# Optimization experiments

Measured on AMD Instinct MI355X. Metric: run time of the kernel, lower is better.

The kernel has to match this reference:

```python
import jax, jax.numpy as jnp
import numpy as np

B, T, C = 2, 4096, 1024
H = 16            # n_head (== n_groups == n_kv_heads)
HD = C // H       # head_dim = 64
W = 256           # window_size
ROPE_BASE = 10000.0


def _rope(x):
    # x: (B, H, T, HD); rotate interleaved pairs with position along axis 2
    t = x.shape[2]
    inv_freq = 1.0 / (ROPE_BASE ** (jnp.arange(0, HD, 2, dtype=jnp.float32) / HD))  # (HD/2,)
    freqs = jnp.arange(t, dtype=jnp.float32)[:, None] * inv_freq[None, :]           # (T, HD/2)
    cos = jnp.cos(freqs)[None, None].astype(x.dtype)
    sin = jnp.sin(freqs)[None, None].astype(x.dtype)
    x1, x2 = x[..., 0::2], x[..., 1::2]
    o1 = x1 * cos - x2 * sin
    o2 = x1 * sin + x2 * cos
    return jnp.stack([o1, o2], axis=-1).reshape(x.shape)


def setup_inputs() -> dict:
    key = jax.random.key(0)
    ks = jax.random.split(key, 5)
    s = 1.0 / np.sqrt(C)
    return {
        "x": jax.random.normal(ks[0], (B, T, C), dtype=jnp.float32),
        "wq": jax.random.normal(ks[1], (C, C), dtype=jnp.float32) * s,
        "wk": jax.random.normal(ks[2], (C, C), dtype=jnp.float32) * s,
        "wv": jax.random.normal(ks[3], (C, C), dtype=jnp.float32) * s,
        "wo": jax.random.normal(ks[4], (C, C), dtype=jnp.float32) * s,
    }


def reference(x, wq, wk, wv, wo):
    # projections (Linear stores (out, in) -> x @ w.T)
    q = jnp.einsum('btc,oc->bto', x, wq).reshape(B, T, H, HD).transpose(0, 2, 1, 3)
    k = jnp.einsum('btc,oc->bto', x, wk).reshape(B, T, H, HD).transpose(0, 2, 1, 3)
    v = jnp.einsum('btc,oc->bto', x, wv).reshape(B, T, H, HD).transpose(0, 2, 1, 3)

    q = _rope(q)
    k = _rope(k)

    nW = T // W
    qw = q.reshape(B, H, nW, W, HD)
    kw = k.reshape(B, H, nW, W, HD)
    vw = v.reshape(B, H, nW, W, HD)

    scale = 1.0 / jnp.sqrt(jnp.asarray(HD, dtype=q.dtype))
    att = jnp.einsum('bhnqd,bhnkd->bhnqk', qw, kw) * scale   # per-window, no causal mask
    att = jax.nn.softmax(att, axis=-1)
    yw = jnp.einsum('bhnqk,bhnkd->bhnqd', att, vw)

    y = yw.reshape(B, H, T, HD).transpose(0, 2, 1, 3).reshape(B, T, C)
    return jnp.einsum('btc,oc->bto', y, wo)
```

## Files before the change

### kernel.cpp

```cpp
#include <hip/hip_runtime.h>
#include <math.h>

typedef float f32x4 __attribute__((ext_vector_type(4)));
typedef __bf16 bf16x8 __attribute__((ext_vector_type(8)));
typedef unsigned short ushort_t;

#define MFMA16(a, b, c) __builtin_amdgcn_mfma_f32_16x16x32_bf16((a), (b), (c), 0, 0, 0)

static __device__ __forceinline__ ushort_t f2bf(float f) {
  union { float f; unsigned u; } v; v.f = f;
  unsigned u = v.u;
  return (ushort_t)((u + 0x7FFFu + ((u >> 16) & 1u)) >> 16);
}
static __device__ __forceinline__ float bf2f(ushort_t h) {
  union { unsigned u; float f; } v; v.u = ((unsigned)h) << 16;
  return v.f;
}
static __device__ __forceinline__ void gl_lds16(const void* g, void* lds_uniform) {
  __builtin_amdgcn_global_load_lds(
      (const __attribute__((address_space(1))) unsigned int*)g,
      (__attribute__((address_space(3))) unsigned int*)lds_uniform, 16, 0, 0);
}

__global__ void prep(const float* __restrict__ x,
                     const float* __restrict__ wq, const float* __restrict__ wk,
                     const float* __restrict__ wv, const float* __restrict__ wo,
                     ushort_t* __restrict__ Xb, ushort_t* __restrict__ Wqb,
                     ushort_t* __restrict__ Wkb, ushort_t* __restrict__ Wvb,
                     ushort_t* __restrict__ Wob, float2* __restrict__ cs) {
  const int bid = blockIdx.x;
  if (bid < 12288) {
    const float* src;
    ushort_t* dst;
    int i;
    if (bid < 8192) {
      src = x; dst = Xb;
      i = bid * 256 + threadIdx.x;
    } else {
      const int wi = (bid - 8192) >> 10;
      src = (wi == 0) ? wq : (wi == 1) ? wk : (wi == 2) ? wv : wo;
      dst = (wi == 0) ? Wqb : (wi == 1) ? Wkb : (wi == 2) ? Wvb : Wob;
      i = ((bid - 8192) & 1023) * 256 + threadIdx.x;
    }
    f32x4 v = ((const f32x4*)src)[i];
    ushort4 o;
    o.x = f2bf(v.x); o.y = f2bf(v.y); o.z = f2bf(v.z); o.w = f2bf(v.w);
    ((ushort4*)dst)[i] = o;
  } else {
    int idx = (bid - 12288) * 256 + threadIdx.x;
    int pos = idx >> 5, i = idx & 31;
    float inv = exp2f(-(float)i * 0.41524101f);
    float th = (float)pos * inv;
    float s, c;
    sincosf(th, &s, &c);
    cs[idx] = make_float2(c, s);
  }
}

template <int OUTBF>
__global__ __launch_bounds__(256) void gemm_nt(
    const ushort_t* __restrict__ A,
    const ushort_t* __restrict__ W0, const ushort_t* __restrict__ W1, const ushort_t* __restrict__ W2,
    void* __restrict__ C0, void* __restrict__ C1, void* __restrict__ C2,
    int K, int N) {
  __shared__ __align__(16) ushort_t As[128 * 64];
  __shared__ __align__(16) ushort_t Bs[128 * 64];
  const int z = blockIdx.z;
  const ushort_t* W = (z == 0) ? W0 : (z == 1 ? W1 : W2);
  void* Cv = (z == 0) ? C0 : (z == 1 ? C1 : C2);

  const int t = threadIdx.x;
  const int lane = t & 63;
  const int l15 = lane & 15;
  const int quad = lane >> 4;
  const int wave = t >> 6;
  const int wm = wave & 1, wn = wave >> 1;
  const int bm = blockIdx.x, bn = blockIdx.y;

  const int srow = t >> 3;
  const int schunk = (t & 7) ^ (srow & 7);
  const ushort_t* Ag = A + (size_t)(bm * 128 + srow) * K + schunk * 8;
  const ushort_t* Wg = W + (size_t)(bn * 128 + srow) * K + schunk * 8;
  char* AsB = (char*)As + (t & 192) * 16;
  char* BsB = (char*)Bs + (t & 192) * 16;
  const size_t rK = (size_t)32 * K;

  const f32x4 zero4 = {0.f, 0.f, 0.f, 0.f};
  f32x4 acc[4][4];
#pragma unroll
  for (int i = 0; i < 4; ++i)
#pragma unroll
    for (int j = 0; j < 4; ++j) acc[i][j] = zero4;

  for (int kt = 0; kt < K; kt += 64) {
#pragma unroll
    for (int p = 0; p < 4; ++p) {
      gl_lds16(Ag + p * rK + kt, AsB + p * 4096);
      gl_lds16(Wg + p * rK + kt, BsB + p * 4096);
    }
    __syncthreads();
#pragma unroll
    for (int ks = 0; ks < 2; ++ks) {
      bf16x8 af[4], bfr[4];
#pragma unroll
      for (int i = 0; i < 4; ++i) {
        const int r = wm * 64 + i * 16 + l15;
        af[i] = *(const bf16x8*)&As[r * 64 + (((ks * 4 + quad) ^ (r & 7)) * 8)];
      }
#pragma unroll
      for (int j = 0; j < 4; ++j) {
        const int r = wn * 64 + j * 16 + l15;
        bfr[j] = *(const bf16x8*)&Bs[r * 64 + (((ks * 4 + quad) ^ (r & 7)) * 8)];
      }
#pragma unroll
      for (int i = 0; i < 4; ++i)
#pragma unroll
        for (int j = 0; j < 4; ++j) acc[i][j] = MFMA16(af[i], bfr[j], acc[i][j]);
    }
    __syncthreads();
  }

  const int rbase = bm * 128 + wm * 64 + quad * 4;
  const int cbase = bn * 128 + wn * 64 + l15;
#pragma unroll
  for (int i = 0; i < 4; ++i)
#pragma unroll
    for (int j = 0; j < 4; ++j)
#pragma unroll
      for (int r = 0; r < 4; ++r) {
        size_t idx = (size_t)(rbase + i * 16 + r) * N + (cbase + j * 16);
        if (OUTBF)
          ((ushort_t*)Cv)[idx] = f2bf(acc[i][j][r]);
        else
          ((float*)Cv)[idx] = acc[i][j][r];
      }
}

static __device__ __forceinline__ void rope8(const ushort_t* __restrict__ g,
                                             ushort_t* __restrict__ lds,
                                             const float2* __restrict__ cs4, float scale) {
  uint4 raw = *(const uint4*)g;
  unsigned rw[4] = {raw.x, raw.y, raw.z, raw.w};
  ushort_t o[8];
#pragma unroll
  for (int m = 0; m < 4; ++m) {
    float x1 = bf2f((ushort_t)(rw[m] & 0xffffu));
    float x2 = bf2f((ushort_t)(rw[m] >> 16));
    float2 sc = cs4[m];
    o[2 * m]     = f2bf((x1 * sc.x - x2 * sc.y) * scale);
    o[2 * m + 1] = f2bf((x1 * sc.y + x2 * sc.x) * scale);
  }
  uint4 w;
  w.x = (unsigned)o[0] | ((unsigned)o[1] << 16);
  w.y = (unsigned)o[2] | ((unsigned)o[3] << 16);
  w.z = (unsigned)o[4] | ((unsigned)o[5] << 16);
  w.w = (unsigned)o[6] | ((unsigned)o[7] << 16);
  *(uint4*)lds = w;
}

static __device__ __forceinline__ bf16x8 rope_frag(const ushort_t* __restrict__ g,
                                                   const float2* __restrict__ cs4,
                                                   float scale) {
  uint4 raw = *(const uint4*)g;
  unsigned rw[4] = {raw.x, raw.y, raw.z, raw.w};
  union { unsigned u[4]; bf16x8 v; } out;
#pragma unroll
  for (int m = 0; m < 4; ++m) {
    float x1 = bf2f((ushort_t)(rw[m] & 0xffffu));
    float x2 = bf2f((ushort_t)(rw[m] >> 16));
    float2 sc = cs4[m];
    float o0 = (x1 * sc.x - x2 * sc.y) * scale;
    float o1 = (x1 * sc.y + x2 * sc.x) * scale;
    out.u[m] = (unsigned)f2bf(o0) | ((unsigned)f2bf(o1) << 16);
  }
  return out.v;
}

__global__ __launch_bounds__(256) void attn(
    const ushort_t* __restrict__ Qb, const ushort_t* __restrict__ Kb,
    const ushort_t* __restrict__ Vb, ushort_t* __restrict__ Yb,
    const float2* __restrict__ cs) {
  __shared__ __align__(16) ushort_t smem[26112];
  ushort_t* Ks = smem;
  ushort_t* Vt = smem;
  ushort_t* Pc = smem + 16896;

  const int t = threadIdx.x;
  const int lane = t & 63, wave = t >> 6;
  const int l15 = lane & 15, quad = lane >> 4;
  const int win = blockIdx.x >> 1, slice = blockIdx.x & 1;
  const int h = blockIdx.y, b = blockIdx.z;
  const int kBase = win * 256, qBase = kBase + slice * 128;
  const size_t gbase = ((size_t)b * 4096) * 1024 + h * 64;

  const int sr = t >> 3;
  const int c0 = (t & 7) * 8;
  const int qw = wave * 32;

#pragma unroll
  for (int p = 0; p < 8; ++p) {
    int r = p * 32 + sr;
    rope8(Kb + gbase + (size_t)(kBase + r) * 1024 + c0, Ks + r * 72 + c0,
          cs + (size_t)(kBase + r) * 32 + (c0 >> 1), 1.0f);
  }

  bf16x8 qf[2][2];
#pragma unroll
  for (int i = 0; i < 2; ++i)
#pragma unroll
    for (int ks = 0; ks < 2; ++ks) {
      int row = qBase + qw + i * 16 + l15;
      int col = ks * 32 + quad * 8;
      qf[i][ks] = rope_frag(Qb + gbase + (size_t)row * 1024 + col,
                            cs + (size_t)row * 32 + (col >> 1), 0.125f);
    }
  __syncthreads();

  uint4 vr[8];
#pragma unroll
  for (int p = 0; p < 8; ++p)
    vr[p] = *(const uint4*)(Vb + gbase + (size_t)(kBase + p * 32 + sr) * 1024 + c0);

  const f32x4 zero4 = {0.f, 0.f, 0.f, 0.f};
  f32x4 ST[2][16];
#pragma unroll
  for (int i = 0; i < 2; ++i)
#pragma unroll
    for (int kt = 0; kt < 16; ++kt) ST[i][kt] = zero4;
#pragma unroll
  for (int ks = 0; ks < 2; ++ks)
#pragma unroll
    for (int kt = 0; kt < 16; ++kt) {
      bf16x8 kf = *(const bf16x8*)&Ks[(kt * 16 + l15) * 72 + ks * 32 + quad * 8];
      ST[0][kt] = MFMA16(kf, qf[0][ks], ST[0][kt]);
      ST[1][kt] = MFMA16(kf, qf[1][ks], ST[1][kt]);
    }

  float mx[2], linv[2];
#pragma unroll
  for (int i = 0; i < 2; ++i) {
    float m = ST[i][0][0];
#pragma unroll
    for (int kt = 0; kt < 16; ++kt)
#pragma unroll
      for (int r = 0; r < 4; ++r) m = fmaxf(m, ST[i][kt][r]);
    m = fmaxf(m, __shfl_xor(m, 16));
    m = fmaxf(m, __shfl_xor(m, 32));
    mx[i] = m;
  }
  unsigned Pp[2][16][2];
#pragma unroll
  for (int i = 0; i < 2; ++i) {
    float sum = 0.f;
#pragma unroll
    for (int kt = 0; kt < 16; ++kt) {
      float e0 = __expf(ST[i][kt][0] - mx[i]);
      float e1 = __expf(ST[i][kt][1] - mx[i]);
      float e2 = __expf(ST[i][kt][2] - mx[i]);
      float e3 = __expf(ST[i][kt][3] - mx[i]);
      sum += (e0 + e1) + (e2 + e3);
      Pp[i][kt][0] = (unsigned)f2bf(e0) | ((unsigned)f2bf(e1) << 16);
      Pp[i][kt][1] = (unsigned)f2bf(e2) | ((unsigned)f2bf(e3) << 16);
    }
    sum += __shfl_xor(sum, 16);
    sum += __shfl_xor(sum, 32);
    linv[i] = 1.0f / sum;
  }

  __syncthreads();

#pragma unroll
  for (int p = 0; p < 8; ++p) {
    int k = p * 32 + sr;
    ushort_t vv[8];
    vv[0] = vr[p].x & 0xffffu; vv[1] = vr[p].x >> 16;
    vv[2] = vr[p].y & 0xffffu; vv[3] = vr[p].y >> 16;
    vv[4] = vr[p].z & 0xffffu; vv[5] = vr[p].z >> 16;
    vv[6] = vr[p].w & 0xffffu; vv[7] = vr[p].w >> 16;
#pragma unroll
    for (int e = 0; e < 8; ++e) {
      int ee = (e + (t & 7)) & 7;
      Vt[(c0 + ee) * 264 + k] = vv[ee];
    }
  }

  auto writeP = [&](int kc) {
#pragma unroll
    for (int i = 0; i < 2; ++i)
#pragma unroll
      for (int jt = 0; jt < 4; ++jt) {
        uint2 w = make_uint2(Pp[i][kc * 4 + jt][0], Pp[i][kc * 4 + jt][1]);
        *(uint2*)&Pc[(qw + i * 16 + l15) * 72 + jt * 16 + quad * 4] = w;
      }
  };

  writeP(0);
  __syncthreads();

  f32x4 O[2][4];
#pragma unroll
  for (int i = 0; i < 2; ++i)
#pragma unroll
    for (int jd = 0; jd < 4; ++jd) O[i][jd] = zero4;

#pragma unroll
  for (int kc = 0; kc < 4; ++kc) {
#pragma unroll
    for (int ks = 0; ks < 2; ++ks) {
      bf16x8 a0 = *(const bf16x8*)&Pc[(qw + l15) * 72 + ks * 32 + quad * 8];
      bf16x8 a1 = *(const bf16x8*)&Pc[(qw + 16 + l15) * 72 + ks * 32 + quad * 8];
#pragma unroll
      for (int jd = 0; jd < 4; ++jd) {
        bf16x8 bv = *(const bf16x8*)&Vt[(jd * 16 + l15) * 264 + kc * 64 + ks * 32 + quad * 8];
        O[0][jd] = MFMA16(a0, bv, O[0][jd]);
        O[1][jd] = MFMA16(a1, bv, O[1][jd]);
      }
    }
    if (kc < 3) writeP(kc + 1);
  }

  float lv[2][4];
#pragma unroll
  for (int i = 0; i < 2; ++i)
#pragma unroll
    for (int r = 0; r < 4; ++r) lv[i][r] = __shfl(linv[i], quad * 4 + r);
#pragma unroll
  for (int i = 0; i < 2; ++i)
#pragma unroll
    for (int jd = 0; jd < 4; ++jd)
#pragma unroll
      for (int r = 0; r < 4; ++r) {
        int row = qBase + qw + i * 16 + quad * 4 + r;
        int col = jd * 16 + l15;
        Yb[gbase + (size_t)row * 1024 + col] = f2bf(O[i][jd][r] * lv[i][r]);
      }
}

extern "C" void kernel_launch(void* const* d_in, const int* in_sizes, int n_in,
                              void* d_out, int out_size, void* d_ws, size_t ws_size,
                              hipStream_t stream) {
  (void)in_sizes; (void)n_in; (void)out_size; (void)ws_size;
  const float* x  = (const float*)d_in[0];
  const float* wq = (const float*)d_in[1];
  const float* wk = (const float*)d_in[2];
  const float* wv = (const float*)d_in[3];
  const float* wo = (const float*)d_in[4];

  char* ws = (char*)d_ws;
  ushort_t* Xb  = (ushort_t*)(ws);
  ushort_t* Wqb = (ushort_t*)(ws + 16777216);
  ushort_t* Wkb = Wqb + 1048576;
  ushort_t* Wvb = Wkb + 1048576;
  ushort_t* Wob = Wvb + 1048576;
  ushort_t* Qb  = (ushort_t*)(ws + 25165824);
  ushort_t* Kb  = Qb + 8388608;
  ushort_t* Vb  = Kb + 8388608;
  ushort_t* Yb  = Vb + 8388608;
  float2*   cs  = (float2*)(ws + 92274688);

  prep<<<dim3(12800), dim3(256), 0, stream>>>(x, wq, wk, wv, wo,
                                              Xb, Wqb, Wkb, Wvb, Wob, cs);

  gemm_nt<1><<<dim3(64, 8, 3), dim3(256), 0, stream>>>(
      Xb, Wqb, Wkb, Wvb, (void*)Qb, (void*)Kb, (void*)Vb, 1024, 1024);

  attn<<<dim3(32, 16, 2), dim3(256), 0, stream>>>(Qb, Kb, Vb, Yb, cs);

  gemm_nt<0><<<dim3(64, 8, 1), dim3(256), 0, stream>>>(
      Yb, Wob, Wob, Wob, d_out, d_out, d_out, 1024, 1024);
}
```

Baseline: 220.4 us.

## Split attention work across 8 waves with 16 query rows each

The attention kernel now launches 512 threads per block, so each wave handles 16 query rows instead of 32. This halves per-thread register state (score tiles, P fragments, accumulators) and the per-thread K/V load and rope work. The V global loads are also moved after the softmax so the V registers are not live during the QK phase. The intent is more waves in flight to hide latency, at the cost of more barrier participants and less reuse of each K/V fragment per wave.

```diff
diff --git a/kernel.cpp b/kernel.cpp
--- a/kernel.cpp
+++ b/kernel.cpp
@@ -176,7 +176,7 @@
   return out.v;
 }
 
-__global__ __launch_bounds__(256) void attn(
+__global__ __launch_bounds__(512, 4) void attn(
     const ushort_t* __restrict__ Qb, const ushort_t* __restrict__ Kb,
     const ushort_t* __restrict__ Vb, ushort_t* __restrict__ Yb,
     const float2* __restrict__ cs) {
@@ -195,83 +195,72 @@
 
   const int sr = t >> 3;
   const int c0 = (t & 7) * 8;
-  const int qw = wave * 32;
-
-#pragma unroll
-  for (int p = 0; p < 8; ++p) {
-    int r = p * 32 + sr;
+  const int qw = wave * 16;
+
+#pragma unroll
+  for (int p = 0; p < 4; ++p) {
+    int r = p * 64 + sr;
     rope8(Kb + gbase + (size_t)(kBase + r) * 1024 + c0, Ks + r * 72 + c0,
           cs + (size_t)(kBase + r) * 32 + (c0 >> 1), 1.0f);
   }
 
-  bf16x8 qf[2][2];
-#pragma unroll
-  for (int i = 0; i < 2; ++i)
-#pragma unroll
-    for (int ks = 0; ks < 2; ++ks) {
-      int row = qBase + qw + i * 16 + l15;
-      int col = ks * 32 + quad * 8;
-      qf[i][ks] = rope_frag(Qb + gbase + (size_t)row * 1024 + col,
-                            cs + (size_t)row * 32 + (col >> 1), 0.125f);
-    }
+  bf16x8 qf[2];
+#pragma unroll
+  for (int ks = 0; ks < 2; ++ks) {
+    int row = qBase + qw + l15;
+    int col = ks * 32 + quad * 8;
+    qf[ks] = rope_frag(Qb + gbase + (size_t)row * 1024 + col,
+                       cs + (size_t)row * 32 + (col >> 1), 0.125f);
+  }
   __syncthreads();
 
-  uint4 vr[8];
-#pragma unroll
-  for (int p = 0; p < 8; ++p)
-    vr[p] = *(const uint4*)(Vb + gbase + (size_t)(kBase + p * 32 + sr) * 1024 + c0);
-
   const f32x4 zero4 = {0.f, 0.f, 0.f, 0.f};
-  f32x4 ST[2][16];
-#pragma unroll
-  for (int i = 0; i < 2; ++i)
-#pragma unroll
-    for (int kt = 0; kt < 16; ++kt) ST[i][kt] = zero4;
+  f32x4 ST[16];
+#pragma unroll
+  for (int kt = 0; kt < 16; ++kt) ST[kt] = zero4;
 #pragma unroll
   for (int ks = 0; ks < 2; ++ks)
 #pragma unroll
     for (int kt = 0; kt < 16; ++kt) {
       bf16x8 kf = *(const bf16x8*)&Ks[(kt * 16 + l15) * 72 + ks * 32 + quad * 8];
-      ST[0][kt] = MFMA16(kf, qf[0][ks], ST[0][kt]);
-      ST[1][kt] = MFMA16(kf, qf[1][ks], ST[1][kt]);
-    }
-
-  float mx[2], linv[2];
-#pragma unroll
-  for (int i = 0; i < 2; ++i) {
-    float m = ST[i][0][0];
-#pragma unroll
-    for (int kt = 0; kt < 16; ++kt)
-#pragma unroll
-      for (int r = 0; r < 4; ++r) m = fmaxf(m, ST[i][kt][r]);
-    m = fmaxf(m, __shfl_xor(m, 16));
-    m = fmaxf(m, __shfl_xor(m, 32));
-    mx[i] = m;
-  }
-  unsigned Pp[2][16][2];
-#pragma unroll
-  for (int i = 0; i < 2; ++i) {
-    float sum = 0.f;
-#pragma unroll
-    for (int kt = 0; kt < 16; ++kt) {
-      float e0 = __expf(ST[i][kt][0] - mx[i]);
-      float e1 = __expf(ST[i][kt][1] - mx[i]);
-      float e2 = __expf(ST[i][kt][2] - mx[i]);
-      float e3 = __expf(ST[i][kt][3] - mx[i]);
-      sum += (e0 + e1) + (e2 + e3);
-      Pp[i][kt][0] = (unsigned)f2bf(e0) | ((unsigned)f2bf(e1) << 16);
-      Pp[i][kt][1] = (unsigned)f2bf(e2) | ((unsigned)f2bf(e3) << 16);
-    }
-    sum += __shfl_xor(sum, 16);
-    sum += __shfl_xor(sum, 32);
-    linv[i] = 1.0f / sum;
-  }
+      ST[kt] = MFMA16(kf, qf[ks], ST[kt]);
+    }
+
+  float m = ST[0][0];
+#pragma unroll
+  for (int kt = 0; kt < 16; ++kt)
+#pragma unroll
+    for (int r = 0; r < 4; ++r) m = fmaxf(m, ST[kt][r]);
+  m = fmaxf(m, __shfl_xor(m, 16));
+  m = fmaxf(m, __shfl_xor(m, 32));
+
+  unsigned Pp[16][2];
+  float sum = 0.f;
+#pragma unroll
+  for (int kt = 0; kt < 16; ++kt) {
+    float e0 = __expf(ST[kt][0] - m);
+    float e1 = __expf(ST[kt][1] - m);
+    float e2 = __expf(ST[kt][2] - m);
+    float e3 = __expf(ST[kt][3] - m);
+    sum += (e0 + e1) + (e2 + e3);
+    Pp[kt][0] = (unsigned)f2bf(e0) | ((unsigned)f2bf(e1) << 16);
+    Pp[kt][1] = (unsigned)f2bf(e2) | ((unsigned)f2bf(e3) << 16);
+  }
+
+  uint4 vr[4];
+#pragma unroll
+  for (int p = 0; p < 4; ++p)
+    vr[p] = *(const uint4*)(Vb + gbase + (size_t)(kBase + p * 64 + sr) * 1024 + c0);
+
+  sum += __shfl_xor(sum, 16);
+  sum += __shfl_xor(sum, 32);
+  const float linv = 1.0f / sum;
 
   __syncthreads();
 
 #pragma unroll
-  for (int p = 0; p < 8; ++p) {
-    int k = p * 32 + sr;
+  for (int p = 0; p < 4; ++p) {
+    int k = p * 64 + sr;
     ushort_t vv[8];
     vv[0] = vr[p].x & 0xffffu; vv[1] = vr[p].x >> 16;
     vv[2] = vr[p].y & 0xffffu; vv[3] = vr[p].y >> 16;
@@ -286,54 +275,44 @@
 
   auto writeP = [&](int kc) {
 #pragma unroll
-    for (int i = 0; i < 2; ++i)
-#pragma unroll
-      for (int jt = 0; jt < 4; ++jt) {
-        uint2 w = make_uint2(Pp[i][kc * 4 + jt][0], Pp[i][kc * 4 + jt][1]);
-        *(uint2*)&Pc[(qw + i * 16 + l15) * 72 + jt * 16 + quad * 4] = w;
-      }
+    for (int jt = 0; jt < 4; ++jt) {
+      uint2 w = make_uint2(Pp[kc * 4 + jt][0], Pp[kc * 4 + jt][1]);
+      *(uint2*)&Pc[(qw + l15) * 72 + jt * 16 + quad * 4] = w;
+    }
   };
 
   writeP(0);
   __syncthreads();
 
-  f32x4 O[2][4];
-#pragma unroll
-  for (int i = 0; i < 2; ++i)
-#pragma unroll
-    for (int jd = 0; jd < 4; ++jd) O[i][jd] = zero4;
+  f32x4 O[4];
+#pragma unroll
+  for (int jd = 0; jd < 4; ++jd) O[jd] = zero4;
 
 #pragma unroll
   for (int kc = 0; kc < 4; ++kc) {
 #pragma unroll
     for (int ks = 0; ks < 2; ++ks) {
       bf16x8 a0 = *(const bf16x8*)&Pc[(qw + l15) * 72 + ks * 32 + quad * 8];
-      bf16x8 a1 = *(const bf16x8*)&Pc[(qw + 16 + l15) * 72 + ks * 32 + quad * 8];
 #pragma unroll
       for (int jd = 0; jd < 4; ++jd) {
         bf16x8 bv = *(const bf16x8*)&Vt[(jd * 16 + l15) * 264 + kc * 64 + ks * 32 + quad * 8];
-        O[0][jd] = MFMA16(a0, bv, O[0][jd]);
-        O[1][jd] = MFMA16(a1, bv, O[1][jd]);
+        O[jd] = MFMA16(a0, bv, O[jd]);
       }
     }
     if (kc < 3) writeP(kc + 1);
   }
 
-  float lv[2][4];
-#pragma unroll
-  for (int i = 0; i < 2; ++i)
-#pragma unroll
-    for (int r = 0; r < 4; ++r) lv[i][r] = __shfl(linv[i], quad * 4 + r);
-#pragma unroll
-  for (int i = 0; i < 2; ++i)
-#pragma unroll
-    for (int jd = 0; jd < 4; ++jd)
-#pragma unroll
-      for (int r = 0; r < 4; ++r) {
-        int row = qBase + qw + i * 16 + quad * 4 + r;
-        int col = jd * 16 + l15;
-        Yb[gbase + (size_t)row * 1024 + col] = f2bf(O[i][jd][r] * lv[i][r]);
-      }
+  float lv[4];
+#pragma unroll
+  for (int r = 0; r < 4; ++r) lv[r] = __shfl(linv, quad * 4 + r);
+#pragma unroll
+  for (int jd = 0; jd < 4; ++jd)
+#pragma unroll
+    for (int r = 0; r < 4; ++r) {
+      int row = qBase + qw + quad * 4 + r;
+      int col = jd * 16 + l15;
+      Yb[gbase + (size_t)row * 1024 + col] = f2bf(O[jd][r] * lv[r]);
+    }
 }
 
 extern "C" void kernel_launch(void* const* d_in, const int* in_sizes, int n_in,
@@ -364,7 +343,7 @@
   gemm_nt<1><<<dim3(64, 8, 3), dim3(256), 0, stream>>>(
       Xb, Wqb, Wkb, Wvb, (void*)Qb, (void*)Kb, (void*)Vb, 1024, 1024);
 
-  attn<<<dim3(32, 16, 2), dim3(256), 0, stream>>>(Qb, Kb, Vb, Yb, cs);
+  attn<<<dim3(32, 16, 2), dim3(512), 0, stream>>>(Qb, Kb, Vb, Yb, cs);
 
   gemm_nt<0><<<dim3(64, 8, 1), dim3(256), 0, stream>>>(
       Yb, Wob, Wob, Wob, d_out, d_out, d_out, 1024, 1024);
```

Result: faster. 210.1 us (-4.7%).
